# Kernel tuning notes

Hardware: AMD Instinct MI355X
Metric: run time of the kernel (lower is better)

## Reference

```python
import jax, jax.numpy as jnp
import numpy as np

B, L, D = 4, 4096, 1024
H, M = 16, 256
DH = D // H  # 64


def setup_inputs() -> dict:
    key = jax.random.key(0)
    ks = jax.random.split(key, 7)
    s = 1.0 / np.sqrt(D).astype(np.float32)  # keep activations O(1) so exp() stays sane
    x = jax.random.normal(ks[0], (B, L, D), dtype=jnp.float32)
    Wq = jax.random.normal(ks[1], (D, D), dtype=jnp.float32) * s
    Wk = jax.random.normal(ks[2], (D, D), dtype=jnp.float32) * s
    Wv = jax.random.normal(ks[3], (D, D), dtype=jnp.float32) * s
    Wo = jax.random.normal(ks[4], (D, D), dtype=jnp.float32) * s
    bo = jnp.zeros((D,), dtype=jnp.float32)
    omega = jax.random.normal(ks[5], (DH, M), dtype=jnp.float32)
    return {"x": x, "Wq": Wq, "Wk": Wk, "Wv": Wv, "Wo": Wo, "bo": bo, "omega": omega}


def _phi(x, omega):
    # x: (B,H,L,dh) -> positive random features (B,H,L,m)
    scale = DH ** 0.25
    x_s = x / scale
    proj = jnp.einsum('bhld,dm->bhlm', x_s, omega)
    norm_sq = jnp.sum(x_s * x_s, axis=-1, keepdims=True) * 0.5
    return jnp.exp(proj - norm_sq) / (M ** 0.5)


def reference(x, Wq, Wk, Wv, Wo, bo, omega):
    # nn.Linear: y = x @ W.T
    def heads(W):
        return (x @ W.T).reshape(B, L, H, DH).transpose(0, 2, 1, 3)
    Q, K, V = heads(Wq), heads(Wk), heads(Wv)
    Q_feat = _phi(Q, omega)   # (B,H,L,m)
    K_feat = _phi(K, omega)   # (B,H,L,m)
    KV = jnp.einsum('bhlm,bhld->bhmd', K_feat, V)      # (B,H,m,dh)
    out = jnp.einsum('bhlm,bhmd->bhld', Q_feat, KV)    # (B,H,L,dh)
    K_sum = K_feat.sum(axis=2)                          # (B,H,m)
    norm = jnp.einsum('bhlm,bhm->bhl', Q_feat, K_sum)
    norm = jnp.clip(norm, 1e-6, None)[..., None]
    out = out / norm
    out = out.transpose(0, 2, 1, 3).reshape(B, L, D)
    return out @ Wo.T + bo
```

## Files before the change

kernel.cpp:

```cpp
#include <hip/hip_runtime.h>

typedef unsigned short u16;
typedef __attribute__((ext_vector_type(4))) float f32x4;
typedef _Float16 f16x8 __attribute__((ext_vector_type(8)));
typedef __attribute__((ext_vector_type(4))) u16   u16x4;
typedef __attribute__((ext_vector_type(8))) u16   u16x8;

#define DEV static __device__ __forceinline__

constexpr int Ll = 4096;

DEV float h2f(u16 v) { _Float16 h; __builtin_memcpy(&h, &v, 2); return (float)h; }
DEV u16 f2h(float f) { _Float16 h = (_Float16)f; u16 u; __builtin_memcpy(&u, &h, 2); return u; }

DEV f32x4 mfma16h(f16x8 a, f16x8 b, f32x4 c) {
    return __builtin_amdgcn_mfma_f32_16x16x32_f16(a, b, c, 0, 0, 0);
}

#if defined(__has_builtin)
#if __has_builtin(__builtin_amdgcn_global_load_lds)
#define HAS_GLLDS 1
#endif
#endif
#ifndef HAS_GLLDS
#define HAS_GLLDS 0
#endif

#define SBAR()  __builtin_amdgcn_s_barrier()
#define SCHED() __builtin_amdgcn_sched_barrier(0)
#define LGKM0() asm volatile("s_waitcnt lgkmcnt(0)" ::: "memory")

#if HAS_GLLDS
#define STG2(BUF, REG, SRC, ROWBASE, TK, KS)                                         \
  { _Pragma("unroll") for (int u_ = 0; u_ < 2; u_++) {                               \
      int row_ = u_ * 128 + wave * 16 + (lane >> 2);                                 \
      int c_ = lane & 3;                                                             \
      const u16* gp_ = (SRC) + (size_t)((ROWBASE) + row_) * 1024 + (TK) * 64         \
                        + (KS) * 32 + ((c_ ^ ((row_ >> 1) & 3)) * 8);                \
      __builtin_amdgcn_global_load_lds(                                              \
        (const __attribute__((address_space(1))) unsigned int*)gp_,                  \
        (__attribute__((address_space(3))) unsigned int*)(sm + (BUF) * 32768 +       \
          (REG) * 8192 + (u_ * 512 + wave * 64) * 8), 16, 0, 0); } }
#else
#define STG2(BUF, REG, SRC, ROWBASE, TK, KS)                                         \
  { _Pragma("unroll") for (int u_ = 0; u_ < 2; u_++) {                               \
      int row_ = u_ * 128 + wave * 16 + (lane >> 2);                                 \
      int c_ = lane & 3;                                                             \
      const u16* gp_ = (SRC) + (size_t)((ROWBASE) + row_) * 1024 + (TK) * 64         \
                        + (KS) * 32 + ((c_ ^ ((row_ >> 1) & 3)) * 8);                \
      *(u16x8*)(sm + (BUF) * 32768 + (REG) * 8192 + (u_ * 512 + wave * 64 + lane) * 8) \
          = *(const u16x8*)gp_; } }
#endif

#if HAS_GLLDS
#define STG(BUF, U, SRC, ROWBASE, KK)                                                \
  { int rl_ = wave * 16 + (lane >> 2);                                               \
    int c_ = lane & 3;                                                               \
    int grow_ = (((U) & 1) * 128) + rl_;                                             \
    const u16* gp_ = (SRC) + (size_t)((ROWBASE) + grow_) * 1024 + (KK)               \
                     + ((c_ ^ ((rl_ >> 1) & 3)) * 8);                                \
    __builtin_amdgcn_global_load_lds(                                                \
        (const __attribute__((address_space(1))) unsigned int*)gp_,                  \
        (__attribute__((address_space(3))) unsigned int*)(sm + (BUF) * 16384 +       \
            (U) * 4096 + wave * 512), 16, 0, 0); }
#else
#define STG(BUF, U, SRC, ROWBASE, KK)                                                \
  { int rl_ = wave * 16 + (lane >> 2);                                               \
    int c_ = lane & 3;                                                               \
    int grow_ = (((U) & 1) * 128) + rl_;                                             \
    const u16* gp_ = (SRC) + (size_t)((ROWBASE) + grow_) * 1024 + (KK)               \
                     + ((c_ ^ ((rl_ >> 1) & 3)) * 8);                                \
    *(u16x8*)(sm + (BUF) * 16384 + (U) * 4096 + wave * 512 + lane * 8)               \
        = *(const u16x8*)gp_; }
#endif

__global__ __launch_bounds__(256) void k_half(const float* __restrict__ s, u16* __restrict__ d) {
    size_t i = ((size_t)blockIdx.x * 256 + threadIdx.x) * 4;
    f32x4 v = *(const f32x4*)(s + i);
    u16x4 h;
#pragma unroll
    for (int j = 0; j < 4; j++) h[j] = f2h(v[j]);
    *(u16x4*)(d + i) = h;
}

__global__ __launch_bounds__(256) void k_halfw(const float* __restrict__ a, const float* __restrict__ b,
                                               const float* __restrict__ c, const float* __restrict__ d2,
                                               u16* __restrict__ o) {
    int y = blockIdx.y;
    const float* src = (y == 0) ? a : (y == 1) ? b : (y == 2) ? c : d2;
    size_t i = ((size_t)blockIdx.x * 256 + threadIdx.x) * 4;
    f32x4 v = *(const f32x4*)(src + i);
    u16x4 h;
#pragma unroll
    for (int j = 0; j < 4; j++) h[j] = f2h(v[j]);
    *(u16x4*)(o + (size_t)y * 1048576 + i) = h;
}

__global__ __launch_bounds__(256) void k_omega(const float* __restrict__ om, u16* __restrict__ wh) {
    int i = blockIdx.x * 256 + threadIdx.x;
    int m = i >> 6, d = i & 63;
    wh[i] = f2h(om[d * 256 + m] * 0.35355339059327373f);
}

__global__ __launch_bounds__(256) void k_zero(float* __restrict__ p, int n) {
    int i = (blockIdx.x * 256 + threadIdx.x) * 4;
    if (i < n) { f32x4 z; z[0]=0.f; z[1]=0.f; z[2]=0.f; z[3]=0.f; *(f32x4*)(p + i) = z; }
}

__global__ __launch_bounds__(512, 1) void k_gemm_qkv(
    const u16* __restrict__ Ax, const u16* __restrict__ Bw,
    u16* __restrict__ QK, u16* __restrict__ Vb) {
    __shared__ __align__(16) u16 sm[65536];
    const int tid = threadIdx.x, wave = tid >> 6, lane = tid & 63;
    const int lr = lane & 15, lkq = lane >> 4;
    const int wr = wave >> 2, wc = wave & 3;
    const int m0 = blockIdx.y * 256, n0 = blockIdx.x * 256;
    const int sec = n0 >> 10;

    const int arow = wr * 128 + lr;
    const int aBase = arow * 32 + ((lkq ^ ((arow >> 1) & 3)) * 8);
    const int brow = wc * 64 + lr;
    const int bBase = 16384 + brow * 32 + ((lkq ^ ((brow >> 1) & 3)) * 8);

    f32x4 acc[8][4];
#pragma unroll
    for (int i = 0; i < 8; i++)
#pragma unroll
        for (int j = 0; j < 4; j++)
#pragma unroll
            for (int r = 0; r < 4; r++) acc[i][j][r] = 0.f;

    STG2(0, 0, Ax, m0, 0, 0)
    STG2(0, 2, Bw, n0, 0, 0)
    STG2(0, 1, Ax, m0, 0, 1)
    STG2(0, 3, Bw, n0, 0, 1)
    asm volatile("s_waitcnt vmcnt(4)" ::: "memory");
    SCHED(); SBAR(); SCHED();

    f16x8 bfr[2][4], afr[4];
    for (int t = 0; t < 16; ++t) {
        const u16* bp = sm + (t & 1) * 32768;
        const int nb = (t + 1) & 1;
        const bool st = t < 15;
#pragma unroll
        for (int f = 0; f < 4; f++) afr[f] = *(const f16x8*)&bp[aBase + f * 512];
#pragma unroll
        for (int j = 0; j < 4; j++) bfr[0][j] = *(const f16x8*)&bp[bBase + j * 512];
        if (st) STG2(nb, 0, Ax, m0, t + 1, 0)
        SBAR(); LGKM0(); SCHED();
        __builtin_amdgcn_s_setprio(1);
#pragma unroll
        for (int i = 0; i < 4; i++)
#pragma unroll
            for (int j = 0; j < 4; j++)
                acc[i][j] = mfma16h(afr[i], bfr[0][j], acc[i][j]);
        __builtin_amdgcn_s_setprio(0);
        SCHED();
        if (st) { asm volatile("s_waitcnt vmcnt(2)" ::: "memory"); }
        else    { asm volatile("s_waitcnt vmcnt(0)" ::: "memory"); }
        SCHED(); SBAR(); SCHED();
#pragma unroll
        for (int f = 0; f < 4; f++) afr[f] = *(const f16x8*)&bp[aBase + 8192 + f * 512];
#pragma unroll
        for (int j = 0; j < 4; j++) bfr[1][j] = *(const f16x8*)&bp[bBase + 8192 + j * 512];
        if (st) STG2(nb, 2, Bw, n0, t + 1, 0)
        SBAR(); LGKM0(); SCHED();
        __builtin_amdgcn_s_setprio(1);
#pragma unroll
        for (int i = 0; i < 4; i++)
#pragma unroll
            for (int j = 0; j < 4; j++)
                acc[i][j] = mfma16h(afr[i], bfr[1][j], acc[i][j]);
        __builtin_amdgcn_s_setprio(0);
        SCHED(); SBAR(); SCHED();
#pragma unroll
        for (int f = 0; f < 4; f++) afr[f] = *(const f16x8*)&bp[aBase + 2048 + f * 512];
        if (st) STG2(nb, 1, Ax, m0, t + 1, 1)
        SBAR(); LGKM0(); SCHED();
        __builtin_amdgcn_s_setprio(1);
#pragma unroll
        for (int i = 0; i < 4; i++)
#pragma unroll
            for (int j = 0; j < 4; j++)
                acc[4 + i][j] = mfma16h(afr[i], bfr[0][j], acc[4 + i][j]);
        __builtin_amdgcn_s_setprio(0);
        SCHED(); SBAR(); SCHED();
#pragma unroll
        for (int f = 0; f < 4; f++) afr[f] = *(const f16x8*)&bp[aBase + 8192 + 2048 + f * 512];
        if (st) STG2(nb, 3, Bw, n0, t + 1, 1)
        SBAR(); LGKM0(); SCHED();
        __builtin_amdgcn_s_setprio(1);
#pragma unroll
        for (int i = 0; i < 4; i++)
#pragma unroll
            for (int j = 0; j < 4; j++)
                acc[4 + i][j] = mfma16h(afr[i], bfr[1][j], acc[4 + i][j]);
        __builtin_amdgcn_s_setprio(0);
        SCHED();
        if (st) { asm volatile("s_waitcnt vmcnt(4)" ::: "memory"); }
        SCHED(); SBAR(); SCHED();
    }

    float* ep = (float*)sm;
    for (int g = 0; g < 8; g++) {
        __syncthreads();
        if (wr == (g >> 2)) {
#pragma unroll
            for (int fi = 0; fi < 2; fi++) {
                int fm = (g & 3) * 2 + fi;
#pragma unroll
                for (int fn = 0; fn < 4; fn++)
#pragma unroll
                    for (int r = 0; r < 4; r++)
                        ep[(fi * 16 + (lane >> 4) * 4 + r) * 264 + wc * 64 + fn * 16 + lr] = acc[fm][fn][r];
            }
        }
        __syncthreads();
        int row = tid >> 4, c0 = (tid & 15) * 16;
        int grow = m0 + g * 32 + row;
        u16x8 h0, h1;
#pragma unroll
        for (int j = 0; j < 8; j++) {
            h0[j] = f2h(ep[row * 264 + c0 + j]);
            h1[j] = f2h(ep[row * 264 + c0 + 8 + j]);
        }
        if (sec < 2) {
            size_t o = (size_t)grow * 2048 + (n0 + c0);
            *(u16x8*)(QK + o) = h0; *(u16x8*)(QK + o + 8) = h1;
        } else {
            size_t o = (size_t)grow * 1024 + (n0 - 2048 + c0);
            *(u16x8*)(Vb + o) = h0; *(u16x8*)(Vb + o + 8) = h1;
        }
    }
}

__global__ __launch_bounds__(512, 2) void k_gemm_out(
    const u16* __restrict__ Ab, const u16* __restrict__ Bw,
    const float* __restrict__ bias, float* __restrict__ outp) {
    __shared__ __align__(16) u16 sm[32768];
    const int tid = threadIdx.x, wave = tid >> 6, lane = tid & 63;
    const int lr = lane & 15, lkq = lane >> 4;
    const int wr = wave >> 2, wc = wave & 3;
    const int m0 = blockIdx.y * 256, n0 = blockIdx.x * 256;

    int aoff[8], boff[4];
#pragma unroll
    for (int f = 0; f < 8; f++) {
        int row = wr * 128 + f * 16 + lr;
        aoff[f] = row * 32 + ((lkq ^ ((row >> 1) & 3)) * 8);
    }
#pragma unroll
    for (int f = 0; f < 4; f++) {
        int row = wc * 64 + f * 16 + lr;
        boff[f] = row * 32 + ((lkq ^ ((row >> 1) & 3)) * 8);
    }

    f32x4 acc[8][4];
#pragma unroll
    for (int i = 0; i < 8; i++)
#pragma unroll
        for (int j = 0; j < 4; j++)
#pragma unroll
            for (int r = 0; r < 4; r++) acc[i][j][r] = 0.f;

    STG(0, 0, Ab, m0, 0) STG(0, 1, Ab, m0, 0)
    STG(0, 2, Bw, n0, 0) STG(0, 3, Bw, n0, 0)
    asm volatile("s_waitcnt vmcnt(0)" ::: "memory");
    SCHED(); SBAR(); SCHED();

    int cb = 0;
    for (int t = 0; t < 32; ++t) {
        const u16* Abase = sm + cb * 16384;
        const u16* Bbase = Abase + 8192;
        f16x8 afr[4], bfr[4];
#pragma unroll
        for (int f = 0; f < 4; f++) bfr[f] = *(const f16x8*)&Bbase[boff[f]];
#pragma unroll
        for (int f = 0; f < 4; f++) afr[f] = *(const f16x8*)&Abase[aoff[f]];
        if (t < 31) {
            int kk = (t + 1) * 32;
            STG(cb ^ 1, 0, Ab, m0, kk) STG(cb ^ 1, 1, Ab, m0, kk)
            STG(cb ^ 1, 2, Bw, n0, kk) STG(cb ^ 1, 3, Bw, n0, kk)
        }
        SCHED(); SBAR(); LGKM0(); SCHED();
        __builtin_amdgcn_s_setprio(1);
#pragma unroll
        for (int i = 0; i < 4; i++)
#pragma unroll
            for (int j = 0; j < 4; j++)
                acc[i][j] = mfma16h(afr[i], bfr[j], acc[i][j]);
        __builtin_amdgcn_s_setprio(0);
        SCHED(); SBAR(); SCHED();
#pragma unroll
        for (int f = 0; f < 4; f++) afr[f] = *(const f16x8*)&Abase[aoff[4 + f]];
        SCHED(); SBAR(); LGKM0(); SCHED();
        __builtin_amdgcn_s_setprio(1);
#pragma unroll
        for (int i = 0; i < 4; i++)
#pragma unroll
            for (int j = 0; j < 4; j++)
                acc[4 + i][j] = mfma16h(afr[i], bfr[j], acc[4 + i][j]);
        __builtin_amdgcn_s_setprio(0);
        asm volatile("s_waitcnt vmcnt(0)" ::: "memory");
        SCHED(); SBAR(); SCHED();
        cb ^= 1;
    }

    float* ep = (float*)sm;
    for (int g = 0; g < 8; g++) {
        __syncthreads();
        if (wr == (g >> 2)) {
#pragma unroll
            for (int fi = 0; fi < 2; fi++) {
                int fm = (g & 3) * 2 + fi;
#pragma unroll
                for (int fn = 0; fn < 4; fn++)
#pragma unroll
                    for (int r = 0; r < 4; r++)
                        ep[(fi * 16 + (lane >> 4) * 4 + r) * 264 + wc * 64 + fn * 16 + lr] = acc[fm][fn][r];
            }
        }
        __syncthreads();
        int row = tid >> 4, c0 = (tid & 15) * 16;
        int grow = m0 + g * 32 + row;
        float vv[16];
#pragma unroll
        for (int j = 0; j < 16; j++) vv[j] = ep[row * 264 + c0 + j] + bias[n0 + c0 + j];
#pragma unroll
        for (int p = 0; p < 4; p++) {
            f32x4 tv;
#pragma unroll
            for (int q = 0; q < 4; q++) tv[q] = vv[p * 4 + q];
            *(f32x4*)(outp + (size_t)grow * 1024 + n0 + c0 + p * 4) = tv;
        }
    }
}

__global__ __launch_bounds__(256) void k_phik_kv(
    const u16* __restrict__ QK, const u16* __restrict__ wt,
    const u16* __restrict__ Vb, float* __restrict__ KVacc, float* __restrict__ Ksum) {
    __shared__ __align__(16) u16 sKh[64 * 72];
    __shared__ __align__(16) u16 sVt[64 * 72];
    __shared__ __align__(16) u16 sKfT[256 * 72];
    __shared__ float snsq[64];
    const int tid = threadIdx.x, wave = tid >> 6, lane = tid & 63;
    const int lr = lane & 15, lk = (lane >> 4) * 8;
    const int kc = blockIdx.x, bh = blockIdx.y;
    const int b = bh >> 4, h = bh & 15;

    f16x8 wb[4][2];
#pragma unroll
    for (int fn = 0; fn < 4; fn++)
#pragma unroll
        for (int ks = 0; ks < 2; ks++)
            wb[fn][ks] = *(const f16x8*)(wt + (size_t)(wave * 64 + fn * 16 + lr) * 64 + ks * 32 + lk);

    f32x4 akv[4][4];
#pragma unroll
    for (int i = 0; i < 4; i++)
#pragma unroll
        for (int j = 0; j < 4; j++)
#pragma unroll
            for (int r = 0; r < 4; r++) akv[i][j][r] = 0.f;
    float ksm[4] = {0.f, 0.f, 0.f, 0.f};

    for (int it = 0; it < 4; it++) {
        int l0 = kc * 256 + it * 64;
        __syncthreads();
        {
            int row = tid >> 2, c0 = (tid & 3) * 16;
            size_t g = ((size_t)(b * Ll + l0 + row)) * 2048 + 1024 + h * 64 + c0;
            u16x8 h0 = *(const u16x8*)(QK + g);
            u16x8 h1 = *(const u16x8*)(QK + g + 8);
            *(u16x8*)&sKh[row * 72 + c0]     = h0;
            *(u16x8*)&sKh[row * 72 + c0 + 8] = h1;
            float s = 0.f;
#pragma unroll
            for (int j = 0; j < 8; j++) {
                float a = h2f(h0[j]); s += a * a;
                float c = h2f(h1[j]); s += c * c;
            }
            s += __shfl_xor(s, 1); s += __shfl_xor(s, 2);
            if ((tid & 3) == 0) snsq[row] = s * 0.0625f;
        }
        {
            int l = tid >> 2, d0 = (tid & 3) * 16;
            size_t g = ((size_t)(b * Ll + l0 + l)) * 1024 + h * 64 + d0;
            u16x8 v0 = *(const u16x8*)(Vb + g);
            u16x8 v1 = *(const u16x8*)(Vb + g + 8);
#pragma unroll
            for (int j = 0; j < 8; j++) {
                sVt[(d0 + j) * 72 + l] = v0[j];
                sVt[(d0 + 8 + j) * 72 + l] = v1[j];
            }
        }
        __syncthreads();
#pragma unroll
        for (int fm = 0; fm < 4; fm++) {
            f32x4 ap[4];
#pragma unroll
            for (int fn = 0; fn < 4; fn++)
#pragma unroll
                for (int r = 0; r < 4; r++) ap[fn][r] = 0.f;
#pragma unroll
            for (int ks = 0; ks < 2; ks++) {
                f16x8 aH = *(const f16x8*)&sKh[(fm * 16 + lr) * 72 + ks * 32 + lk];
#pragma unroll
                for (int fn = 0; fn < 4; fn++)
                    ap[fn] = mfma16h(aH, wb[fn][ks], ap[fn]);
            }
#pragma unroll
            for (int fn = 0; fn < 4; fn++) {
                u16x4 pk;
#pragma unroll
                for (int r = 0; r < 4; r++) {
                    float ns = snsq[fm * 16 + (lane >> 4) * 4 + r];
                    float val = __expf(ap[fn][r] - ns) * 0.00390625f;
                    ksm[fn] += val;
                    pk[r] = f2h(val);
                }
                *(u16x4*)&sKfT[(wave * 64 + fn * 16 + lr) * 72 + fm * 16 + (lane >> 4) * 4] = pk;
            }
        }
#pragma unroll
        for (int ks = 0; ks < 2; ks++) {
            f16x8 a4[4], b4[4];
#pragma unroll
            for (int f = 0; f < 4; f++) {
                a4[f] = *(const f16x8*)&sKfT[(wave * 64 + f * 16 + lr) * 72 + ks * 32 + lk];
                b4[f] = *(const f16x8*)&sVt[(f * 16 + lr) * 72 + ks * 32 + lk];
            }
#pragma unroll
            for (int fm = 0; fm < 4; fm++)
#pragma unroll
                for (int fn = 0; fn < 4; fn++)
                    akv[fm][fn] = mfma16h(a4[fm], b4[fn], akv[fm][fn]);
        }
    }
#pragma unroll
    for (int fm = 0; fm < 4; fm++)
#pragma unroll
        for (int fn = 0; fn < 4; fn++)
#pragma unroll
            for (int r = 0; r < 4; r++) {
                int m = wave * 64 + fm * 16 + (lane >> 4) * 4 + r;
                int d = fn * 16 + lr;
                atomicAdd(&KVacc[((size_t)bh << 14) + m * 64 + d], akv[fm][fn][r]);
            }
#pragma unroll
    for (int fn = 0; fn < 4; fn++) {
        ksm[fn] += __shfl_xor(ksm[fn], 16);
        ksm[fn] += __shfl_xor(ksm[fn], 32);
    }
    if (lane < 16) {
#pragma unroll
        for (int fn = 0; fn < 4; fn++)
            atomicAdd(&Ksum[bh * 256 + wave * 64 + fn * 16 + lane], ksm[fn]);
    }
}

__global__ __launch_bounds__(256) void k_kvt(const float* __restrict__ KVacc, u16* __restrict__ KVt) {
    int i = blockIdx.x * 256 + threadIdx.x;
    int bh = i >> 14, dd = (i >> 8) & 63, m = i & 255;
    KVt[i] = f2h(KVacc[((size_t)bh << 14) + m * 64 + dd]);
}

__global__ __launch_bounds__(512) void k_phiq_attn(
    const u16* __restrict__ QK, const u16* __restrict__ wt,
    const u16* __restrict__ KVt, const float* __restrict__ Ksum,
    u16* __restrict__ attn) {
    __shared__ __align__(16) u16 sQh[64 * 72];
    __shared__ __align__(16) u16 sQf[64 * 264];
    __shared__ float sKs[256];
    __shared__ float snsq[64];
    __shared__ float snorm[64];
    const int tid = threadIdx.x, wave = tid >> 6, lane = tid & 63;
    const int lr = lane & 15, lk = (lane >> 4) * 8;
    const int bh = blockIdx.y, b = bh >> 4, h = bh & 15;
    const int mq = wave & 3;
    const int lh = wave >> 2;
    const int af = wave & 3;
    const int ad = wave >> 2;

    f16x8 wb[4][2];
#pragma unroll
    for (int fn = 0; fn < 4; fn++)
#pragma unroll
        for (int ks = 0; ks < 2; ks++)
            wb[fn][ks] = *(const f16x8*)(wt + (size_t)(mq * 64 + fn * 16 + lr) * 64 + ks * 32 + lk);
    f16x8 kvb[2][8];
#pragma unroll
    for (int fn = 0; fn < 2; fn++)
#pragma unroll
        for (int ks = 0; ks < 8; ks++)
            kvb[fn][ks] = *(const f16x8*)(KVt + ((size_t)bh << 14) +
                                          (size_t)(ad * 32 + fn * 16 + lr) * 256 + ks * 32 + lk);
    if (tid < 256) sKs[tid] = Ksum[bh * 256 + tid];

    for (int st = 0; st < 2; st++) {
        const int l0 = (blockIdx.x * 2 + st) * 64;
        __syncthreads();
        {
            int row = tid >> 3, c0 = (tid & 7) * 8;
            size_t g = ((size_t)(b * Ll + l0 + row)) * 2048 + h * 64 + c0;
            u16x8 vh = *(const u16x8*)(QK + g);
            *(u16x8*)&sQh[row * 72 + c0] = vh;
            float s = 0.f;
#pragma unroll
            for (int j = 0; j < 8; j++) { float a = h2f(vh[j]); s += a * a; }
            s += __shfl_xor(s, 1); s += __shfl_xor(s, 2); s += __shfl_xor(s, 4);
            if ((tid & 7) == 0) snsq[row] = s * 0.0625f;
        }
        __syncthreads();
#pragma unroll
        for (int fm = 0; fm < 2; fm++) {
            f32x4 ap[4];
#pragma unroll
            for (int fn = 0; fn < 4; fn++)
#pragma unroll
                for (int r = 0; r < 4; r++) ap[fn][r] = 0.f;
#pragma unroll
            for (int ks = 0; ks < 2; ks++) {
                f16x8 aH = *(const f16x8*)&sQh[(lh * 32 + fm * 16 + lr) * 72 + ks * 32 + lk];
#pragma unroll
                for (int fn = 0; fn < 4; fn++)
                    ap[fn] = mfma16h(aH, wb[fn][ks], ap[fn]);
            }
#pragma unroll
            for (int fn = 0; fn < 4; fn++)
#pragma unroll
                for (int r = 0; r < 4; r++) {
                    int l = lh * 32 + fm * 16 + (lane >> 4) * 4 + r;
                    int m = mq * 64 + fn * 16 + lr;
                    sQf[l * 264 + m] = f2h(__expf(ap[fn][r] - snsq[l]) * 0.0625f);
                }
        }
        __syncthreads();
        {
            int l = tid >> 3, m0 = (tid & 7) * 32;
            float s = 0.f;
#pragma unroll
            for (int j4 = 0; j4 < 4; j4++) {
                u16x8 qv = *(const u16x8*)&sQf[l * 264 + m0 + j4 * 8];
#pragma unroll
                for (int j = 0; j < 8; j++) s += h2f(qv[j]) * sKs[m0 + j4 * 8 + j];
            }
            s += __shfl_xor(s, 1); s += __shfl_xor(s, 2); s += __shfl_xor(s, 4);
            if ((tid & 7) == 0) snorm[l] = s;
        }
        f32x4 aa[2];
#pragma unroll
        for (int fn = 0; fn < 2; fn++)
#pragma unroll
            for (int r = 0; r < 4; r++) aa[fn][r] = 0.f;
#pragma unroll
        for (int ks = 0; ks < 8; ks++) {
            f16x8 a = *(const f16x8*)&sQf[(af * 16 + lr) * 264 + ks * 32 + lk];
            aa[0] = mfma16h(a, kvb[0][ks], aa[0]);
            aa[1] = mfma16h(a, kvb[1][ks], aa[1]);
        }
        __syncthreads();
        float* ep = (float*)sQf;
#pragma unroll
        for (int fn = 0; fn < 2; fn++)
#pragma unroll
            for (int r = 0; r < 4; r++) {
                int l = af * 16 + (lane >> 4) * 4 + r;
                int d = ad * 32 + fn * 16 + lr;
                ep[l * 68 + d] = aa[fn][r];
            }
        __syncthreads();
        {
            int l = tid >> 3, d0 = (tid & 7) * 8;
            float inv = 1.0f / fmaxf(snorm[l], 6.25e-8f);
            u16x8 o;
#pragma unroll
            for (int j = 0; j < 8; j++) o[j] = f2h(ep[l * 68 + d0 + j] * inv);
            *(u16x8*)(attn + ((size_t)(b * Ll + l0 + l)) * 1024 + h * 64 + d0) = o;
        }
    }
}

extern "C" void kernel_launch(void* const* d_in, const int* in_sizes, int n_in,
                              void* d_out, int out_size, void* d_ws, size_t ws_size,
                              hipStream_t stream) {
    (void)in_sizes; (void)n_in; (void)out_size; (void)ws_size;
    const float* x  = (const float*)d_in[0];
    const float* Wq = (const float*)d_in[1];
    const float* Wk = (const float*)d_in[2];
    const float* Wv = (const float*)d_in[3];
    const float* Wo = (const float*)d_in[4];
    const float* bo = (const float*)d_in[5];
    const float* om = (const float*)d_in[6];

    char* w = (char*)d_ws;
    size_t o = 0;
    auto take = [&](size_t n) { char* p = w + o; o += n; return p; };
    u16* QK  = (u16*)take(67108864);
    u16* Vb  = (u16*)take(33554432);
    u16* xh  = (u16*)take(33554432);
    u16* Wc  = (u16*)take(6291456);
    u16* Wof = (u16*)take(2097152);
    u16* wt  = (u16*)take(32768);
    float* KVacc = (float*)take(4194304);
    float* Ksum  = (float*)take(65536);
    u16* KVt = (u16*)take(2097152);
    u16* attn = Vb;

    k_half<<<16384, 256, 0, stream>>>(x, xh);
    k_halfw<<<dim3(1024, 4), 256, 0, stream>>>(Wq, Wk, Wv, Wo, Wc);
    k_omega<<<64, 256, 0, stream>>>(om, wt);
    k_zero<<<1040, 256, 0, stream>>>(KVacc, 1064960);

    k_gemm_qkv<<<dim3(12, 64), 512, 0, stream>>>(xh, Wc, QK, Vb);
    k_phik_kv<<<dim3(16, 64), 256, 0, stream>>>(QK, wt, Vb, KVacc, Ksum);
    k_kvt<<<4096, 256, 0, stream>>>(KVacc, KVt);
    k_phiq_attn<<<dim3(32, 64), 512, 0, stream>>>(QK, wt, KVt, Ksum, attn);
    k_gemm_out<<<dim3(4, 64), 512, 0, stream>>>(attn, Wof, bo, (float*)d_out);
}
```

Measured before the change: 406.4 us.

## Fuse prep kernels, replace KV atomics with partial sums, prefetch tiles

Merges the x, weight and omega conversion kernels into one launch and drops the zeroing kernel. The phi(K)·V kernel now writes per-chunk partial KV and Ksum instead of using atomics, with k_kvt reducing the 8 chunks. The phik_kv and phiq_attn kernels process more rows per block and register-prefetch the next tile's global loads. This removes launches and atomic contention but adds a larger partial buffer and extra reduction traffic, and halves grid sizes.

```diff
diff --git a/kernel.cpp b/kernel.cpp
--- a/kernel.cpp
+++ b/kernel.cpp
@@ -74,37 +74,32 @@
         = *(const u16x8*)gp_; }
 #endif
 
-__global__ __launch_bounds__(256) void k_half(const float* __restrict__ s, u16* __restrict__ d) {
-    size_t i = ((size_t)blockIdx.x * 256 + threadIdx.x) * 4;
-    f32x4 v = *(const f32x4*)(s + i);
-    u16x4 h;
-#pragma unroll
-    for (int j = 0; j < 4; j++) h[j] = f2h(v[j]);
-    *(u16x4*)(d + i) = h;
-}
-
-__global__ __launch_bounds__(256) void k_halfw(const float* __restrict__ a, const float* __restrict__ b,
-                                               const float* __restrict__ c, const float* __restrict__ d2,
-                                               u16* __restrict__ o) {
-    int y = blockIdx.y;
-    const float* src = (y == 0) ? a : (y == 1) ? b : (y == 2) ? c : d2;
-    size_t i = ((size_t)blockIdx.x * 256 + threadIdx.x) * 4;
-    f32x4 v = *(const f32x4*)(src + i);
-    u16x4 h;
-#pragma unroll
-    for (int j = 0; j < 4; j++) h[j] = f2h(v[j]);
-    *(u16x4*)(o + (size_t)y * 1048576 + i) = h;
-}
-
-__global__ __launch_bounds__(256) void k_omega(const float* __restrict__ om, u16* __restrict__ wh) {
-    int i = blockIdx.x * 256 + threadIdx.x;
-    int m = i >> 6, d = i & 63;
-    wh[i] = f2h(om[d * 256 + m] * 0.35355339059327373f);
-}
-
-__global__ __launch_bounds__(256) void k_zero(float* __restrict__ p, int n) {
-    int i = (blockIdx.x * 256 + threadIdx.x) * 4;
-    if (i < n) { f32x4 z; z[0]=0.f; z[1]=0.f; z[2]=0.f; z[3]=0.f; *(f32x4*)(p + i) = z; }
+__global__ __launch_bounds__(256) void k_prep(
+    const float* __restrict__ x, const float* __restrict__ Wq, const float* __restrict__ Wk,
+    const float* __restrict__ Wv, const float* __restrict__ Wo, const float* __restrict__ om,
+    u16* __restrict__ xh, u16* __restrict__ Wc, u16* __restrict__ wtp) {
+    int bx = blockIdx.x, tid = threadIdx.x;
+    if (bx < 16384) {
+        size_t i = ((size_t)bx * 256 + tid) * 4;
+        f32x4 v = *(const f32x4*)(x + i);
+        u16x4 h;
+#pragma unroll
+        for (int j = 0; j < 4; j++) h[j] = f2h(v[j]);
+        *(u16x4*)(xh + i) = h;
+    } else if (bx < 20480) {
+        int wsel = (bx - 16384) >> 10;
+        const float* src = (wsel == 0) ? Wq : (wsel == 1) ? Wk : (wsel == 2) ? Wv : Wo;
+        size_t i = ((size_t)((bx - 16384) & 1023) * 256 + tid) * 4;
+        f32x4 v = *(const f32x4*)(src + i);
+        u16x4 h;
+#pragma unroll
+        for (int j = 0; j < 4; j++) h[j] = f2h(v[j]);
+        *(u16x4*)(Wc + (size_t)wsel * 1048576 + i) = h;
+    } else {
+        int i = (bx - 20480) * 256 + tid;
+        int m = i >> 6, d = i & 63;
+        wtp[i] = f2h(om[d * 256 + m] * 0.35355339059327373f);
+    }
 }
 
 __global__ __launch_bounds__(512, 1) void k_gemm_qkv(
@@ -364,37 +359,43 @@
             for (int r = 0; r < 4; r++) akv[i][j][r] = 0.f;
     float ksm[4] = {0.f, 0.f, 0.f, 0.f};
 
-    for (int it = 0; it < 4; it++) {
-        int l0 = kc * 256 + it * 64;
+    const int rowS = tid >> 2, cS = (tid & 3) * 16;
+    size_t gK = ((size_t)(b * Ll + kc * 512 + rowS)) * 2048 + 1024 + h * 64 + cS;
+    size_t gV = ((size_t)(b * Ll + kc * 512 + rowS)) * 1024 + h * 64 + cS;
+    u16x8 kh0 = *(const u16x8*)(QK + gK);
+    u16x8 kh1 = *(const u16x8*)(QK + gK + 8);
+    u16x8 vv0 = *(const u16x8*)(Vb + gV);
+    u16x8 vv1 = *(const u16x8*)(Vb + gV + 8);
+
+    for (int it = 0; it < 8; it++) {
         __syncthreads();
         {
-            int row = tid >> 2, c0 = (tid & 3) * 16;
-            size_t g = ((size_t)(b * Ll + l0 + row)) * 2048 + 1024 + h * 64 + c0;
-            u16x8 h0 = *(const u16x8*)(QK + g);
-            u16x8 h1 = *(const u16x8*)(QK + g + 8);
-            *(u16x8*)&sKh[row * 72 + c0]     = h0;
-            *(u16x8*)&sKh[row * 72 + c0 + 8] = h1;
+            *(u16x8*)&sKh[rowS * 72 + cS]     = kh0;
+            *(u16x8*)&sKh[rowS * 72 + cS + 8] = kh1;
             float s = 0.f;
 #pragma unroll
             for (int j = 0; j < 8; j++) {
-                float a = h2f(h0[j]); s += a * a;
-                float c = h2f(h1[j]); s += c * c;
+                float a = h2f(kh0[j]); s += a * a;
+                float c = h2f(kh1[j]); s += c * c;
             }
             s += __shfl_xor(s, 1); s += __shfl_xor(s, 2);
-            if ((tid & 3) == 0) snsq[row] = s * 0.0625f;
+            if ((tid & 3) == 0) snsq[rowS] = s * 0.0625f;
         }
         {
-            int l = tid >> 2, d0 = (tid & 3) * 16;
-            size_t g = ((size_t)(b * Ll + l0 + l)) * 1024 + h * 64 + d0;
-            u16x8 v0 = *(const u16x8*)(Vb + g);
-            u16x8 v1 = *(const u16x8*)(Vb + g + 8);
 #pragma unroll
             for (int j = 0; j < 8; j++) {
-                sVt[(d0 + j) * 72 + l] = v0[j];
-                sVt[(d0 + 8 + j) * 72 + l] = v1[j];
-            }
-        }
-        __syncthreads();
+                sVt[(cS + j) * 72 + rowS]     = vv0[j];
+                sVt[(cS + 8 + j) * 72 + rowS] = vv1[j];
+            }
+        }
+        __syncthreads();
+        if (it < 7) {
+            gK += 131072; gV += 65536;
+            kh0 = *(const u16x8*)(QK + gK);
+            kh1 = *(const u16x8*)(QK + gK + 8);
+            vv0 = *(const u16x8*)(Vb + gV);
+            vv1 = *(const u16x8*)(Vb + gV + 8);
+        }
 #pragma unroll
         for (int fm = 0; fm < 4; fm++) {
             f32x4 ap[4];
@@ -437,6 +438,7 @@
                     akv[fm][fn] = mfma16h(a4[fm], b4[fn], akv[fm][fn]);
         }
     }
+    const size_t base = ((size_t)(kc * 64 + bh)) << 14;
 #pragma unroll
     for (int fm = 0; fm < 4; fm++)
 #pragma unroll
@@ -445,7 +447,7 @@
             for (int r = 0; r < 4; r++) {
                 int m = wave * 64 + fm * 16 + (lane >> 4) * 4 + r;
                 int d = fn * 16 + lr;
-                atomicAdd(&KVacc[((size_t)bh << 14) + m * 64 + d], akv[fm][fn][r]);
+                KVacc[base + m * 64 + d] = akv[fm][fn][r];
             }
 #pragma unroll
     for (int fn = 0; fn < 4; fn++) {
@@ -455,14 +457,30 @@
     if (lane < 16) {
 #pragma unroll
         for (int fn = 0; fn < 4; fn++)
-            atomicAdd(&Ksum[bh * 256 + wave * 64 + fn * 16 + lane], ksm[fn]);
-    }
-}
-
-__global__ __launch_bounds__(256) void k_kvt(const float* __restrict__ KVacc, u16* __restrict__ KVt) {
+            Ksum[(kc * 64 + bh) * 256 + wave * 64 + fn * 16 + lane] = ksm[fn];
+    }
+}
+
+__global__ __launch_bounds__(256) void k_kvt(const float* __restrict__ KVacc,
+                                             const float* __restrict__ Ksum,
+                                             u16* __restrict__ KVt, float* __restrict__ KsumR) {
     int i = blockIdx.x * 256 + threadIdx.x;
-    int bh = i >> 14, dd = (i >> 8) & 63, m = i & 255;
-    KVt[i] = f2h(KVacc[((size_t)bh << 14) + m * 64 + dd]);
+    if (blockIdx.x < 16384) {
+        int bh = i >> 14, m = (i >> 6) & 255, d = i & 63;
+        float s = 0.f;
+#pragma unroll
+        for (int kc = 0; kc < 8; kc++)
+            s += KVacc[(((size_t)(kc * 64 + bh)) << 14) + m * 64 + d];
+        KVt[((size_t)bh << 14) + d * 256 + m] = f2h(s);
+    } else {
+        int j = i - 4194304;
+        int bh = j >> 8, m = j & 255;
+        float s = 0.f;
+#pragma unroll
+        for (int kc = 0; kc < 8; kc++)
+            s += Ksum[(kc * 64 + bh) * 256 + m];
+        KsumR[j] = s;
+    }
 }
 
 __global__ __launch_bounds__(512) void k_phiq_attn(
@@ -497,19 +515,20 @@
                                           (size_t)(ad * 32 + fn * 16 + lr) * 256 + ks * 32 + lk);
     if (tid < 256) sKs[tid] = Ksum[bh * 256 + tid];
 
-    for (int st = 0; st < 2; st++) {
-        const int l0 = (blockIdx.x * 2 + st) * 64;
+    const int rowQ = tid >> 3, cQ = (tid & 7) * 8;
+    size_t gQ = ((size_t)(b * Ll + blockIdx.x * 256 + rowQ)) * 2048 + h * 64 + cQ;
+    u16x8 vh = *(const u16x8*)(QK + gQ);
+
+    for (int st = 0; st < 4; st++) {
+        const int l0 = blockIdx.x * 256 + st * 64;
         __syncthreads();
         {
-            int row = tid >> 3, c0 = (tid & 7) * 8;
-            size_t g = ((size_t)(b * Ll + l0 + row)) * 2048 + h * 64 + c0;
-            u16x8 vh = *(const u16x8*)(QK + g);
-            *(u16x8*)&sQh[row * 72 + c0] = vh;
+            *(u16x8*)&sQh[rowQ * 72 + cQ] = vh;
             float s = 0.f;
 #pragma unroll
             for (int j = 0; j < 8; j++) { float a = h2f(vh[j]); s += a * a; }
             s += __shfl_xor(s, 1); s += __shfl_xor(s, 2); s += __shfl_xor(s, 4);
-            if ((tid & 7) == 0) snsq[row] = s * 0.0625f;
+            if ((tid & 7) == 0) snsq[rowQ] = s * 0.0625f;
         }
         __syncthreads();
 #pragma unroll
@@ -534,6 +553,10 @@
                     int m = mq * 64 + fn * 16 + lr;
                     sQf[l * 264 + m] = f2h(__expf(ap[fn][r] - snsq[l]) * 0.0625f);
                 }
+        }
+        if (st < 3) {
+            gQ += 131072;
+            vh = *(const u16x8*)(QK + gQ);
         }
         __syncthreads();
         {
@@ -599,22 +622,19 @@
     u16* QK  = (u16*)take(67108864);
     u16* Vb  = (u16*)take(33554432);
     u16* xh  = (u16*)take(33554432);
-    u16* Wc  = (u16*)take(6291456);
-    u16* Wof = (u16*)take(2097152);
+    u16* Wc  = (u16*)take(8388608);
     u16* wt  = (u16*)take(32768);
-    float* KVacc = (float*)take(4194304);
-    float* Ksum  = (float*)take(65536);
+    float* KVacc = (float*)take(33554432);
+    float* Ksum  = (float*)take(524288);
+    float* KsumR = (float*)take(65536);
     u16* KVt = (u16*)take(2097152);
+    u16* Wof  = Wc + 3145728;
     u16* attn = Vb;
 
-    k_half<<<16384, 256, 0, stream>>>(x, xh);
-    k_halfw<<<dim3(1024, 4), 256, 0, stream>>>(Wq, Wk, Wv, Wo, Wc);
-    k_omega<<<64, 256, 0, stream>>>(om, wt);
-    k_zero<<<1040, 256, 0, stream>>>(KVacc, 1064960);
-
+    k_prep<<<20544, 256, 0, stream>>>(x, Wq, Wk, Wv, Wo, om, xh, Wc, wt);
     k_gemm_qkv<<<dim3(12, 64), 512, 0, stream>>>(xh, Wc, QK, Vb);
-    k_phik_kv<<<dim3(16, 64), 256, 0, stream>>>(QK, wt, Vb, KVacc, Ksum);
-    k_kvt<<<4096, 256, 0, stream>>>(KVacc, KVt);
-    k_phiq_attn<<<dim3(32, 64), 512, 0, stream>>>(QK, wt, KVt, Ksum, attn);
+    k_phik_kv<<<dim3(8, 64), 256, 0, stream>>>(QK, wt, Vb, KVacc, Ksum);
+    k_kvt<<<16448, 256, 0, stream>>>(KVacc, Ksum, KVt, KsumR);
+    k_phiq_attn<<<dim3(16, 64), 512, 0, stream>>>(QK, wt, KVt, KsumR, attn);
     k_gemm_out<<<dim3(4, 64), 512, 0, stream>>>(attn, Wof, bo, (float*)d_out);
 }
```

After: 369.6 us. 9.1% less time.
